# Kernel optimization log

Hardware: AMD Instinct MI355X
Metric: run time of the kernel (lower is better)

The kernel has to match this reference:

```python
import jax, jax.numpy as jnp
import numpy as np

H = 1024
M = 4096
K = 64            # max_memory_updates_per_step
THRESH = 0.5      # surprise_threshold
EPS = 1e-12


def setup_inputs() -> dict:
    key = jax.random.key(0)
    ks = jax.random.split(key, 5)
    B, S = 4, 2048
    return {
        "hidden_states": jax.random.normal(ks[0], (B, S, H), dtype=jnp.float32),
        "ln_gamma": jnp.ones((H,), jnp.float32),
        "ln_beta": jnp.zeros((H,), jnp.float32),
        "Wq": jax.random.normal(ks[1], (H, H), jnp.float32) * 0.02,
        "bq": jnp.zeros((H,), jnp.float32),
        "Wo": jax.random.normal(ks[2], (H, H), jnp.float32) * 0.02,
        "bo": jnp.zeros((H,), jnp.float32),
        "memory": jax.random.normal(ks[3], (M, H), jnp.float32),
        "importance_scores": jax.random.uniform(ks[4], (M,), jnp.float32),
    }


def _layer_norm(x, g, b):
    mu = jnp.mean(x, axis=-1, keepdims=True)
    var = jnp.mean(jnp.square(x - mu), axis=-1, keepdims=True)
    return (x - mu) * jax.lax.rsqrt(var + EPS) * g + b


def reference(hidden_states, ln_gamma, ln_beta, Wq, bq, Wo, bo, memory, importance_scores):
    # LayerNorm
    norm = _layer_norm(hidden_states, ln_gamma, ln_beta)  # [B,S,H]

    # Surprise measure (detached): mean |x| over hidden dim
    surprise = jnp.mean(jnp.abs(jax.lax.stop_gradient(norm)), axis=-1)  # [B,S]

    # --- surprise-based memory update (buffers; no gradient, training mode) ---
    flat_h = jax.lax.stop_gradient(norm).reshape(-1, H)   # [B*S, H]
    flat_s = surprise.reshape(-1)                          # [B*S]
    # top-K surprises, descending (matches where>thr -> sort desc -> take K)
    top_vals, top_idx = jax.lax.top_k(flat_s, K)
    valid = top_vals > THRESH                              # entries below threshold: no write
    # K slots with smallest importance, ascending importance order
    _, slots = jax.lax.top_k(-importance_scores, K)
    new_rows = flat_h[top_idx]                             # [K, H]
    old_rows = memory[slots]                               # [K, H]
    mem = memory.at[slots].set(jnp.where(valid[:, None], new_rows, old_rows))  # [M,H]

    # --- query memory ---
    q = jnp.einsum("bsh,oh->bso", norm, Wq) + bq           # query_proj
    sim = jnp.einsum("bsh,mh->bsm", q, mem)                # [B,S,M]
    attn = jax.nn.softmax(sim, axis=-1)
    retrieved = jnp.einsum("bsm,mh->bsh", attn, mem)       # [B,S,H]
    mem_out = jnp.einsum("bsh,oh->bso", retrieved, Wo) + bo  # output_proj

    # dropout in eval mode = identity; residual add
    return hidden_states + mem_out
```

## Files before the change

### kernel.cpp

```cpp
#include <hip/hip_runtime.h>

#define H 1024
#define MMEM 4096
#define NTOK 8192
#define KTOP 64
#define FTHRESH 0.5f

typedef _Float16 half8 __attribute__((ext_vector_type(8)));
typedef float vf4 __attribute__((ext_vector_type(4)));

__device__ __forceinline__ short f2h(float x){
  union { _Float16 h; short s; } u; u.h = (_Float16)x; return u.s;
}
__device__ __forceinline__ float h2f(short s){
  union { _Float16 h; short s; } u; u.s = s; return (float)u.h;
}
__device__ __forceinline__ unsigned fkey_of(float x){
  unsigned u = __float_as_uint(x);
  return (u & 0x80000000u) ? ~u : (u | 0x80000000u);
}
__device__ __forceinline__ float val_of(unsigned k){
  unsigned u = (k & 0x80000000u) ? (k & 0x7fffffffu) : ~k;
  return __uint_as_float(u);
}

__device__ __forceinline__ void gload_lds16(const short* g, short* l){
  __builtin_amdgcn_global_load_lds(
      (const __attribute__((address_space(1))) unsigned int*)g,
      (__attribute__((address_space(3))) unsigned int*)l, 16, 0, 0);
}

__global__ __launch_bounds__(256) void ln_kernel(
    const float* __restrict__ hs, const float* __restrict__ g, const float* __restrict__ be,
    short* __restrict__ n16, float* __restrict__ surprise)
{
  int row = blockIdx.x, tid = threadIdx.x;
  long base = (long)row * H;
  float4 x = ((const float4*)(hs + base))[tid];
  float s1 = x.x + x.y + x.z + x.w;
  float s2 = x.x*x.x + x.y*x.y + x.z*x.z + x.w*x.w;
  __shared__ float r1[4], r2[4], r3[4];
  int w = tid >> 6, lane = tid & 63;
  for (int o = 32; o; o >>= 1){ s1 += __shfl_down(s1, o); s2 += __shfl_down(s2, o); }
  if (lane == 0){ r1[w] = s1; r2[w] = s2; }
  __syncthreads();
  float S1 = r1[0]+r1[1]+r1[2]+r1[3];
  float S2 = r2[0]+r2[1]+r2[2]+r2[3];
  float mean = S1 * (1.0f/H);
  float var  = S2 * (1.0f/H) - mean*mean;
  float rinv = rsqrtf(var + 1e-12f);
  float4 gg = ((const float4*)g)[tid];
  float4 bb = ((const float4*)be)[tid];
  float4 n;
  n.x = (x.x-mean)*rinv*gg.x + bb.x;
  n.y = (x.y-mean)*rinv*gg.y + bb.y;
  n.z = (x.z-mean)*rinv*gg.z + bb.z;
  n.w = (x.w-mean)*rinv*gg.w + bb.w;
  float sa = fabsf(n.x)+fabsf(n.y)+fabsf(n.z)+fabsf(n.w);
  for (int o = 32; o; o >>= 1) sa += __shfl_down(sa, o);
  if (lane == 0) r3[w] = sa;
  __syncthreads();
  if (tid == 0) surprise[row] = (r3[0]+r3[1]+r3[2]+r3[3]) * (1.0f/H);
  short4 h4;
  h4.x = f2h(n.x); h4.y = f2h(n.y); h4.z = f2h(n.z); h4.w = f2h(n.w);
  ((short4*)(n16 + base))[tid] = h4;
}

__global__ __launch_bounds__(256) void topk_local(
    const float* __restrict__ surprise, const float* __restrict__ imp,
    unsigned long long* __restrict__ cand_s, unsigned long long* __restrict__ cand_i)
{
  __shared__ unsigned long long s[256];
  int b = blockIdx.x, tid = threadIdx.x;
  int maxmode = (b < 32);
  int gidx = maxmode ? (b*256 + tid) : ((b-32)*256 + tid);
  float x = maxmode ? surprise[gidx] : imp[gidx];
  unsigned k = fkey_of(x);
  if (!maxmode) k = ~k;
  s[tid] = ((unsigned long long)k << 32) | (unsigned)(8191 - gidx);
  __syncthreads();
  for (int kk = 2; kk <= 256; kk <<= 1)
    for (int j = kk >> 1; j > 0; j >>= 1){
      int i = tid, ixj = i ^ j;
      if (ixj > i){
        bool asc = ((i & kk) == 0);
        unsigned long long a = s[i], c = s[ixj];
        if ((a < c) == asc){ s[i] = c; s[ixj] = a; }
      }
      __syncthreads();
    }
  if (tid < 64){
    if (maxmode) cand_s[b*64 + tid] = s[tid];
    else         cand_i[(b-32)*64 + tid] = s[tid];
  }
}

__global__ __launch_bounds__(256) void topk_merge(
    const unsigned long long* __restrict__ cand_s, const unsigned long long* __restrict__ cand_i,
    float* __restrict__ top_vals, int* __restrict__ top_idx, int* __restrict__ slots)
{
  __shared__ unsigned long long s[2048];
  int tid = threadIdx.x;
  int N = (blockIdx.x == 0) ? 2048 : 1024;
  const unsigned long long* src = (blockIdx.x == 0) ? cand_s : cand_i;
  for (int i = tid; i < N; i += 256) s[i] = src[i];
  __syncthreads();
  for (int kk = 2; kk <= N; kk <<= 1)
    for (int j = kk >> 1; j > 0; j >>= 1){
      for (int i = tid; i < N; i += 256){
        int ixj = i ^ j;
        if (ixj > i){
          bool asc = ((i & kk) == 0);
          unsigned long long a = s[i], c = s[ixj];
          if ((a < c) == asc){ s[i] = c; s[ixj] = a; }
        }
      }
      __syncthreads();
    }
  if (tid < 64){
    unsigned long long p = s[tid];
    int gi = 8191 - (int)(p & 0xffffffffu);
    if (blockIdx.x == 0){
      top_vals[tid] = val_of((unsigned)(p >> 32));
      top_idx[tid] = gi;
    } else {
      slots[tid] = gi;
    }
  }
}

__global__ __launch_bounds__(256) void prep_all_kernel(
    const float* __restrict__ mem, const float* __restrict__ Wq, const float* __restrict__ Wo,
    const float* __restrict__ bq,
    short* __restrict__ m16, short* __restrict__ wqT, short* __restrict__ wo16,
    float* __restrict__ biasM)
{
  int b = blockIdx.x, tid = threadIdx.x;
  if (b < 4096){
    long i = (long)b * 256 + tid;
    float4 x = ((const float4*)mem)[i];
    short4 h;
    h.x = f2h(x.x); h.y = f2h(x.y); h.z = f2h(x.z); h.w = f2h(x.w);
    ((short4*)m16)[i] = h;
    float4 b4 = ((const float4*)bq)[tid];
    float sb = b4.x*h2f(h.x) + b4.y*h2f(h.y) + b4.z*h2f(h.z) + b4.w*h2f(h.w);
    int wv = tid >> 6, lane = tid & 63;
    for (int o = 32; o; o >>= 1) sb += __shfl_down(sb, o);
    __shared__ float rb_[4];
    if (lane == 0) rb_[wv] = sb;
    __syncthreads();
    if (tid == 0) biasM[b] = rb_[0]+rb_[1]+rb_[2]+rb_[3];
  } else if (b < 5120){
    long i = (long)(b - 4096) * 256 + tid;
    float4 x = ((const float4*)Wo)[i];
    short4 h;
    h.x = f2h(x.x); h.y = f2h(x.y); h.z = f2h(x.z); h.w = f2h(x.w);
    ((short4*)wo16)[i] = h;
  } else {
    __shared__ __align__(16) short t[64][66];
    int tb = b - 5120;
    int r0 = (tb >> 4) * 64, c0 = (tb & 15) * 64;
    #pragma unroll
    for (int k = 0; k < 4; ++k){
      int idx = k*256 + tid;
      int r = idx >> 4, c4 = (idx & 15) * 4;
      float4 x = *(const float4*)&Wq[(long)(r0+r)*H + c0 + c4];
      t[r][c4]   = f2h(x.x);
      t[r][c4+1] = f2h(x.y);
      t[r][c4+2] = f2h(x.z);
      t[r][c4+3] = f2h(x.w);
    }
    __syncthreads();
    #pragma unroll
    for (int k = 0; k < 4; ++k){
      int idx = k*256 + tid;
      int c = idx >> 4, r4 = (idx & 15) * 4;
      short4 h;
      h.x = t[r4][c]; h.y = t[r4+1][c]; h.z = t[r4+2][c]; h.w = t[r4+3][c];
      *(short4*)&wqT[(long)(c0+c)*H + r0 + r4] = h;
    }
  }
}

__global__ __launch_bounds__(256) void update_kernel(
    const float* __restrict__ top_vals, const int* __restrict__ top_idx, const int* __restrict__ slots,
    const float* __restrict__ hs, const float* __restrict__ g, const float* __restrict__ be,
    const float* __restrict__ bq,
    short* __restrict__ m16, float* __restrict__ biasM)
{
  int i = blockIdx.x;
  if (top_vals[i] <= FTHRESH) return;
  int s = slots[i], r = top_idx[i];
  int tid = threadIdx.x, w = tid >> 6, lane = tid & 63;
  long base = (long)r * H;
  float4 x = ((const float4*)(hs + base))[tid];
  float s1 = x.x + x.y + x.z + x.w;
  float s2 = x.x*x.x + x.y*x.y + x.z*x.z + x.w*x.w;
  __shared__ float r1[4], r2[4], rb[4];
  for (int o = 32; o; o >>= 1){ s1 += __shfl_down(s1, o); s2 += __shfl_down(s2, o); }
  if (lane == 0){ r1[w] = s1; r2[w] = s2; }
  __syncthreads();
  float S1 = r1[0]+r1[1]+r1[2]+r1[3];
  float S2 = r2[0]+r2[1]+r2[2]+r2[3];
  float mean = S1 * (1.0f/H);
  float var  = S2 * (1.0f/H) - mean*mean;
  float rinv = rsqrtf(var + 1e-12f);
  float4 gg = ((const float4*)g)[tid];
  float4 bb = ((const float4*)be)[tid];
  short4 h4;
  h4.x = f2h((x.x-mean)*rinv*gg.x + bb.x);
  h4.y = f2h((x.y-mean)*rinv*gg.y + bb.y);
  h4.z = f2h((x.z-mean)*rinv*gg.z + bb.z);
  h4.w = f2h((x.w-mean)*rinv*gg.w + bb.w);
  ((short4*)(m16 + (long)s*H))[tid] = h4;
  float4 b4 = ((const float4*)bq)[tid];
  float sb = b4.x*h2f(h4.x) + b4.y*h2f(h4.y) + b4.z*h2f(h4.z) + b4.w*h2f(h4.w);
  for (int o = 32; o; o >>= 1) sb += __shfl_down(sb, o);
  if (lane == 0) rb[w] = sb;
  __syncthreads();
  if (tid == 0) biasM[s] = rb[0]+rb[1]+rb[2]+rb[3];
}

__global__ __launch_bounds__(256) void gemm_dual(
    const short* __restrict__ A0, const short* __restrict__ B0, int N0, short* __restrict__ O0,
    const short* __restrict__ A1, const short* __restrict__ B1, int N1, short* __restrict__ O1,
    int K)
{
  __shared__ short sA[128*64];
  __shared__ short sB[128*64];
  int tid = threadIdx.x, w = tid >> 6, lane = tid & 63, ln = lane & 15, quad = lane >> 4;
  int wr = w >> 1, wc = w & 1;
  int lin = blockIdx.x;
  int nl  = (lin & 7) * 64 + (lin >> 3);
  int second = (nl >= 256);
  int t = second ? (nl - 256) : nl;
  const short* A = second ? A1 : A0;
  const short* B = second ? B1 : B0;
  short* O = second ? O1 : O0;
  int N = second ? N1 : N0;
  int nwgx = N >> 7;
  long m0 = (long)(t / nwgx) * 128, n0 = (long)(t % nwgx) * 128;
  long Kl = K;
  vf4 acc[4][4];
  #pragma unroll
  for (int i = 0; i < 4; ++i) for (int j = 0; j < 4; ++j) for (int r = 0; r < 4; ++r) acc[i][j][r] = 0.0f;

  for (long kk = 0; kk < Kl; kk += 64){
    #pragma unroll
    for (int j = 0; j < 4; ++j){
      int f = (w*4 + j)*64 + lane;
      int row = f >> 3, c8 = f & 7;
      long go = kk + (long)((c8 ^ (row & 7)) * 8);
      gload_lds16(A + (m0+row)*Kl + go, sA + (w*4+j)*512);
      gload_lds16(B + (n0+row)*Kl + go, sB + (w*4+j)*512);
    }
    __syncthreads();
    #pragma unroll
    for (int ks = 0; ks < 64; ks += 32){
      int cbase = (ks >> 3) + quad;
      half8 bh[4];
      #pragma unroll
      for (int j = 0; j < 4; ++j){
        int rb = wc*64 + j*16 + ln;
        bh[j] = *(const half8*)&sB[rb*64 + (cbase ^ (rb & 7))*8];
      }
      #pragma unroll
      for (int i = 0; i < 4; ++i){
        int ra = wr*64 + i*16 + ln;
        half8 a = *(const half8*)&sA[ra*64 + (cbase ^ (ra & 7))*8];
        #pragma unroll
        for (int j = 0; j < 4; ++j)
          acc[i][j] = __builtin_amdgcn_mfma_f32_16x16x32_f16(a, bh[j], acc[i][j], 0, 0, 0);
      }
    }
    __syncthreads();
  }

  #pragma unroll
  for (int i = 0; i < 4; ++i)
    #pragma unroll
    for (int j = 0; j < 4; ++j)
      #pragma unroll
      for (int r = 0; r < 4; ++r){
        long row = m0 + wr*64 + i*16 + quad*4 + r;
        long col = n0 + wc*64 + j*16 + ln;
        O[row*(long)N + col] = f2h(acc[i][j][r]);
      }
}

template<int MODE>
__global__ __launch_bounds__(512, 2) void gemm256(
    const short* __restrict__ A, const short* __restrict__ B,
    int K, int N,
    short* __restrict__ O1, float* __restrict__ Of,
    const float* __restrict__ resid, const float* __restrict__ biasN)
{
  extern __shared__ short lds[];
  int tid = threadIdx.x, w = tid >> 6, lane = tid & 63, ln = lane & 15, quad = lane >> 4;
  int wr = w >> 2, wc = w & 3;
  int nwgx = gridDim.x, nwg = nwgx * gridDim.y;
  int lin = blockIdx.y * nwgx + blockIdx.x;
  int nl  = (lin & 7) * (nwg >> 3) + (lin >> 3);
  long m0 = (long)(nl / nwgx) * 256, n0 = (long)(nl % nwgx) * 256;
  long Kl = K;
  int NT = K >> 6;

  auto STAGE = [&](const short* __restrict__ G, long rowbase, long kt, short* ldsbase){
    #pragma unroll
    for (int i = 0; i < 2; ++i){
      int f = i*512 + tid;
      int row = f >> 3, c8 = f & 7;
      long go = kt + (long)((c8 ^ (row & 7)) * 8);
      gload_lds16(G + (rowbase + row)*Kl + go, ldsbase + i*4096 + w*512);
    }
  };
  auto LOADA = [&](half8 (&af)[4][2], const short* sAh){
    #pragma unroll
    for (int ks = 0; ks < 2; ++ks){
      int cbase = ks*4 + quad;
      #pragma unroll
      for (int i = 0; i < 4; ++i){
        int ra = wr*64 + i*16 + ln;
        af[i][ks] = *(const half8*)&sAh[ra*64 + (cbase ^ (ra & 7))*8];
      }
    }
  };
  auto LOADB = [&](half8 (&bf)[2][2], const short* sBh){
    #pragma unroll
    for (int ks = 0; ks < 2; ++ks){
      int cbase = ks*4 + quad;
      #pragma unroll
      for (int j = 0; j < 2; ++j){
        int rb = wc*32 + j*16 + ln;
        bf[j][ks] = *(const half8*)&sBh[rb*64 + (cbase ^ (rb & 7))*8];
      }
    }
  };

  vf4 acc[4][4][2];
  #pragma unroll
  for (int p = 0; p < 4; ++p)
    for (int i = 0; i < 4; ++i)
      for (int j = 0; j < 2; ++j)
        for (int r = 0; r < 4; ++r) acc[p][i][j][r] = 0.0f;

  {
    int t1 = (NT > 1) ? 1 : 0;
    STAGE(A, m0 + 0,   0, lds + 0);
    STAGE(B, n0 + 0,   0, lds + 16384);
    STAGE(B, n0 + 128, 0, lds + 16384 + 8192);
    STAGE(A, m0 + 128, 0, lds + 8192);
    STAGE(A, m0 + 0,   (long)t1*64, lds + 32768);
    STAGE(B, n0 + 0,   (long)t1*64, lds + 32768 + 16384);
  }
  asm volatile("s_waitcnt vmcnt(8)" ::: "memory");
  asm volatile("s_barrier" ::: "memory");

  #define PH_MID()  do { \
    asm volatile("s_waitcnt lgkmcnt(0)" ::: "memory"); \
    __builtin_amdgcn_sched_barrier(0); \
    __builtin_amdgcn_s_setprio(1); } while(0)
  #define PH_END() do { \
    __builtin_amdgcn_s_setprio(0); \
    asm volatile("s_waitcnt vmcnt(8)" ::: "memory"); \
    asm volatile("s_barrier" ::: "memory"); } while(0)
  #define MFMA16(ap, af, bf) do { \
    _Pragma("unroll") \
    for (int i = 0; i < 4; ++i){ \
      _Pragma("unroll") \
      for (int j = 0; j < 2; ++j){ \
        ap[i][j] = __builtin_amdgcn_mfma_f32_16x16x32_f16(af[i][0], bf[j][0], ap[i][j], 0, 0, 0); \
        ap[i][j] = __builtin_amdgcn_mfma_f32_16x16x32_f16(af[i][1], bf[j][1], ap[i][j], 0, 0, 0); \
      } \
    } } while(0)

  for (int t = 0; t < NT; ++t){
    int cur = t & 1;
    short* bA = lds + cur*32768;
    short* bB = bA + 16384;
    short* oA = lds + (cur^1)*32768;
    short* oB = oA + 16384;
    int t1 = t + 1; if (t1 >= NT) t1 -= NT;
    int t2 = t + 2; if (t2 >= NT) t2 -= NT;
    long kt1 = (long)t1 * 64, kt2 = (long)t2 * 64;
    half8 af[4][2], bf0[2][2], bf1[2][2];

    LOADA(af, bA);
    LOADB(bf0, bB);
    STAGE(B, n0 + 128, kt1, oB + 8192);
    PH_MID();
    MFMA16(acc[0], af, bf0);
    PH_END();

    LOADB(bf1, bB + 8192);
    STAGE(A, m0 + 128, kt1, oA + 8192);
    PH_MID();
    MFMA16(acc[1], af, bf1);
    PH_END();

    LOADA(af, bA + 8192);
    STAGE(A, m0 + 0, kt2, bA);
    PH_MID();
    MFMA16(acc[2], af, bf0);
    PH_END();

    STAGE(B, n0 + 0, kt2, bB);
    PH_MID();
    MFMA16(acc[3], af, bf1);
    PH_END();
  }
  #undef PH_MID
  #undef PH_END
  #undef MFMA16

  float bn[2][2];
  if (MODE != 2){
    #pragma unroll
    for (int bh = 0; bh < 2; ++bh)
      for (int j = 0; j < 2; ++j)
        bn[bh][j] = biasN[n0 + bh*128 + wc*32 + j*16 + ln];
  }
  #pragma unroll
  for (int p = 0; p < 4; ++p){
    #pragma unroll
    for (int i = 0; i < 4; ++i){
      #pragma unroll
      for (int j = 0; j < 2; ++j){
        #pragma unroll
        for (int r = 0; r < 4; ++r){
          long row = m0 + (p >> 1)*128 + wr*64 + i*16 + quad*4 + r;
          long col = n0 + (p & 1)*128 + wc*32 + j*16 + ln;
          float v = acc[p][i][j][r];
          if (MODE == 1){
            O1[row*(long)N + col] = f2h(v + bn[p & 1][j]);
          } else if (MODE == 2){
            O1[row*(long)N + col] = f2h(v);
          } else {
            Of[row*(long)N + col] = v + resid[row*(long)N + col] + bn[p & 1][j];
          }
        }
      }
    }
  }
}

__global__ __launch_bounds__(512, 2) void gemm_out(
    const short* __restrict__ A, const short* __restrict__ B,
    int K, int N,
    float* __restrict__ Of, const float* __restrict__ resid, const float* __restrict__ biasN)
{
  extern __shared__ short lds[];
  int tid = threadIdx.x, w = tid >> 6, lane = tid & 63, ln = lane & 15, quad = lane >> 4;
  int wr = (w >> 2) & 1, wc = w & 3;
  int nwgx = gridDim.x, nwg = nwgx * gridDim.y;
  int lin = blockIdx.y * nwgx + blockIdx.x;
  int nl  = (lin & 7) * (nwg >> 3) + (lin >> 3);
  long m0 = (long)(nl >> 2) * 128, n0 = (long)(nl & 3) * 256;
  long Kl = K;
  int NT = K >> 6;

  auto STAGE_A = [&](long rowbase, long kt, short* dst){
    int f = tid;
    int row = f >> 3, c8 = f & 7;
    long go = kt + (long)((c8 ^ (row & 7)) * 8);
    gload_lds16(A + (rowbase + row)*Kl + go, dst + w*512);
  };
  auto STAGE_B = [&](long rowbase, long kt, short* dst){
    #pragma unroll
    for (int i = 0; i < 2; ++i){
      int f = i*512 + tid;
      int row = f >> 3, c8 = f & 7;
      long go = kt + (long)((c8 ^ (row & 7)) * 8);
      gload_lds16(B + (rowbase + row)*Kl + go, dst + i*4096 + w*512);
    }
  };
  auto LOADA = [&](half8 (&af)[2][2], const short* sAh){
    #pragma unroll
    for (int ks = 0; ks < 2; ++ks){
      int cbase = ks*4 + quad;
      #pragma unroll
      for (int i = 0; i < 2; ++i){
        int ra = wr*32 + i*16 + ln;
        af[i][ks] = *(const half8*)&sAh[ra*64 + (cbase ^ (ra & 7))*8];
      }
    }
  };
  auto LOADB = [&](half8 (&bf)[2][2], const short* sBh){
    #pragma unroll
    for (int ks = 0; ks < 2; ++ks){
      int cbase = ks*4 + quad;
      #pragma unroll
      for (int j = 0; j < 2; ++j){
        int rb = wc*32 + j*16 + ln;
        bf[j][ks] = *(const half8*)&sBh[rb*64 + (cbase ^ (rb & 7))*8];
      }
    }
  };

  vf4 acc[4][2][2];
  #pragma unroll
  for (int p = 0; p < 4; ++p)
    for (int i = 0; i < 2; ++i)
      for (int j = 0; j < 2; ++j)
        for (int r = 0; r < 4; ++r) acc[p][i][j][r] = 0.0f;

  {
    int t1 = (NT > 1) ? 1 : 0;
    STAGE_A(m0 + 0,   0, lds + 0);
    STAGE_B(n0 + 0,   0, lds + 8192);
    STAGE_B(n0 + 128, 0, lds + 16384);
    STAGE_A(m0 + 64,  0, lds + 4096);
    STAGE_A(m0 + 0,   (long)t1*64, lds + 24576);
    STAGE_B(n0 + 0,   (long)t1*64, lds + 24576+8192);
  }
  asm volatile("s_waitcnt vmcnt(6)" ::: "memory");
  asm volatile("s_barrier" ::: "memory");

  #define FPH_MID()  do { \
    asm volatile("s_waitcnt lgkmcnt(0)" ::: "memory"); \
    __builtin_amdgcn_sched_barrier(0); \
    __builtin_amdgcn_s_setprio(1); } while(0)
  #define FPH_END() do { \
    __builtin_amdgcn_s_setprio(0); \
    asm volatile("s_waitcnt vmcnt(6)" ::: "memory"); \
    asm volatile("s_barrier" ::: "memory"); } while(0)
  #define MFMA8(ap, af, bf) do { \
    _Pragma("unroll") \
    for (int i = 0; i < 2; ++i){ \
      _Pragma("unroll") \
      for (int j = 0; j < 2; ++j){ \
        ap[i][j] = __builtin_amdgcn_mfma_f32_16x16x32_f16(af[i][0], bf[j][0], ap[i][j], 0, 0, 0); \
        ap[i][j] = __builtin_amdgcn_mfma_f32_16x16x32_f16(af[i][1], bf[j][1], ap[i][j], 0, 0, 0); \
      } \
    } } while(0)

  for (int t = 0; t < NT; ++t){
    int cur = t & 1;
    short* bA = lds + cur*24576;
    short* oA = lds + (cur^1)*24576;
    int t1 = t + 1; if (t1 >= NT) t1 -= NT;
    int t2 = t + 2; if (t2 >= NT) t2 -= NT;
    long kt1 = (long)t1 * 64, kt2 = (long)t2 * 64;
    half8 af[2][2], bf0[2][2], bf1[2][2];

    LOADA(af, bA);
    LOADB(bf0, bA + 8192);
    STAGE_B(n0 + 128, kt1, oA + 16384);
    FPH_MID();
    MFMA8(acc[0], af, bf0);
    FPH_END();

    LOADB(bf1, bA + 16384);
    STAGE_A(m0 + 64, kt1, oA + 4096);
    FPH_MID();
    MFMA8(acc[1], af, bf1);
    FPH_END();

    LOADA(af, bA + 4096);
    STAGE_A(m0 + 0, kt2, bA);
    FPH_MID();
    MFMA8(acc[2], af, bf0);
    FPH_END();

    STAGE_B(n0 + 0, kt2, bA + 8192);
    FPH_MID();
    MFMA8(acc[3], af, bf1);
    FPH_END();
  }
  #undef FPH_MID
  #undef FPH_END
  #undef MFMA8

  float bn[2][2];
  #pragma unroll
  for (int bh = 0; bh < 2; ++bh)
    for (int j = 0; j < 2; ++j)
      bn[bh][j] = biasN[n0 + bh*128 + wc*32 + j*16 + ln];
  #pragma unroll
  for (int p = 0; p < 4; ++p){
    #pragma unroll
    for (int i = 0; i < 2; ++i){
      #pragma unroll
      for (int j = 0; j < 2; ++j){
        #pragma unroll
        for (int r = 0; r < 4; ++r){
          long row = m0 + (p >> 1)*64 + wr*32 + i*16 + quad*4 + r;
          long col = n0 + (p & 1)*128 + wc*32 + j*16 + ln;
          Of[row*(long)N + col] = acc[p][i][j][r] + resid[row*(long)N + col] + bn[p & 1][j];
        }
      }
    }
  }
}

__global__ __launch_bounds__(256) void softmax_kernel(short* __restrict__ simP)
{
  long row = blockIdx.x;
  int tid = threadIdx.x, w = tid >> 6, lane = tid & 63;
  half8* ptr = (half8*)(simP + row*MMEM);
  float xf[16];
  float mx = -1e30f;
  #pragma unroll
  for (int j = 0; j < 2; ++j){
    half8 x = ptr[tid + j*256];
    #pragma unroll
    for (int e = 0; e < 8; ++e){ float f = (float)x[e]; xf[j*8+e] = f; mx = fmaxf(mx, f); }
  }
  for (int o = 32; o; o >>= 1) mx = fmaxf(mx, __shfl_xor(mx, o));
  __shared__ float rmax[4], rsum[4];
  if (lane == 0) rmax[w] = mx;
  __syncthreads();
  mx = fmaxf(fmaxf(rmax[0], rmax[1]), fmaxf(rmax[2], rmax[3]));
  float p[16], s = 0.f;
  #pragma unroll
  for (int k = 0; k < 16; ++k){ p[k] = __expf(xf[k] - mx); s += p[k]; }
  for (int o = 32; o; o >>= 1) s += __shfl_xor(s, o);
  if (lane == 0) rsum[w] = s;
  __syncthreads();
  float inv = 1.0f / (rsum[0]+rsum[1]+rsum[2]+rsum[3]);
  #pragma unroll
  for (int j = 0; j < 2; ++j){
    half8 o8;
    #pragma unroll
    for (int e = 0; e < 8; ++e) o8[e] = (_Float16)(p[j*8+e] * inv);
    ptr[tid + j*256] = o8;
  }
}

extern "C" void kernel_launch(void* const* d_in, const int* in_sizes, int n_in,
                              void* d_out, int out_size, void* d_ws, size_t ws_size,
                              hipStream_t stream)
{
  const float* hs  = (const float*)d_in[0];
  const float* gam = (const float*)d_in[1];
  const float* bet = (const float*)d_in[2];
  const float* Wq  = (const float*)d_in[3];
  const float* bq  = (const float*)d_in[4];
  const float* Wo  = (const float*)d_in[5];
  const float* bo  = (const float*)d_in[6];
  const float* mem = (const float*)d_in[7];
  const float* imp = (const float*)d_in[8];
  float* out = (float*)d_out;

  char* ws = (char*)d_ws;
  short* n16   = (short*)(ws);
  short* g16   = (short*)(ws + (16ull<<20));
  short* m16   = (short*)(ws + (32ull<<20));
  short* wqT   = (short*)(ws + (40ull<<20));
  short* simP  = (short*)(ws + (48ull<<20));
  short* vwoT  = (short*)(ws + (112ull<<20));
  short* wo16  = (short*)(ws + (132ull<<20));
  char*  tail  = ws + (134ull<<20);
  float* biasM    = (float*)tail;
  float* surprise = (float*)(tail + (64<<10));
  float* top_vals = (float*)(tail + (128<<10));
  int*   top_idx  = (int*)  (tail + (129<<10));
  int*   slots    = (int*)  (tail + (130<<10));
  unsigned long long* cand_s = (unsigned long long*)(tail + (132<<10));
  unsigned long long* cand_i = (unsigned long long*)(tail + (148<<10));

  static bool attr_done = false;
  if (!attr_done){
    (void)hipFuncSetAttribute(reinterpret_cast<const void*>(&gemm256<1>),
                              hipFuncAttributeMaxDynamicSharedMemorySize, 131072);
    (void)hipFuncSetAttribute(reinterpret_cast<const void*>(&gemm_out),
                              hipFuncAttributeMaxDynamicSharedMemorySize, 98304);
    attr_done = true;
  }

  ln_kernel<<<NTOK, 256, 0, stream>>>(hs, gam, bet, n16, surprise);
  topk_local<<<48, 256, 0, stream>>>(surprise, imp, cand_s, cand_i);
  topk_merge<<<2, 256, 0, stream>>>(cand_s, cand_i, top_vals, top_idx, slots);
  prep_all_kernel<<<5376, 256, 0, stream>>>(mem, Wq, Wo, bq, m16, wqT, wo16, biasM);
  update_kernel<<<KTOP, 256, 0, stream>>>(top_vals, top_idx, slots, hs, gam, bet, bq, m16, biasM);
  gemm_dual<<<512, 256, 0, stream>>>(
      wo16, m16, MMEM, vwoT,  m16, wqT, H, g16,  H);
  gemm256<1><<<dim3(16,32), 512, 131072, stream>>>(
      n16, g16, H, MMEM, simP, nullptr, nullptr, biasM);
  softmax_kernel<<<NTOK, 256, 0, stream>>>(simP);
  gemm_out<<<dim3(4, 64), 512, 98304, stream>>>(
      simP, vwoT, MMEM, H, out, hs, bo);
}
```

Measured before the change: 370.0 us.

## Fuse layernorm and weight-prep kernels; remap gemm256 tiles to XCD-local blocks

Merges the layernorm/surprise kernel and the memory/Wq/Wo fp16 conversion kernel into one launch, dispatching by block index, so one kernel boundary goes away and the two independent streaming jobs can run side by side. It also replaces the gemm256 block remap with an explicit mapping that gives each XCD a contiguous 8x8 group of 256x256 tiles, to improve L2 reuse of the A and B panels. The new mapping hardcodes a 16x32 grid shape.

```diff
diff --git a/kernel.cpp b/kernel.cpp
--- a/kernel.cpp
+++ b/kernel.cpp
@@ -30,40 +30,91 @@
       (__attribute__((address_space(3))) unsigned int*)l, 16, 0, 0);
 }
 
-__global__ __launch_bounds__(256) void ln_kernel(
+__global__ __launch_bounds__(256) void ln_prep_kernel(
     const float* __restrict__ hs, const float* __restrict__ g, const float* __restrict__ be,
-    short* __restrict__ n16, float* __restrict__ surprise)
-{
-  int row = blockIdx.x, tid = threadIdx.x;
-  long base = (long)row * H;
-  float4 x = ((const float4*)(hs + base))[tid];
-  float s1 = x.x + x.y + x.z + x.w;
-  float s2 = x.x*x.x + x.y*x.y + x.z*x.z + x.w*x.w;
-  __shared__ float r1[4], r2[4], r3[4];
-  int w = tid >> 6, lane = tid & 63;
-  for (int o = 32; o; o >>= 1){ s1 += __shfl_down(s1, o); s2 += __shfl_down(s2, o); }
-  if (lane == 0){ r1[w] = s1; r2[w] = s2; }
-  __syncthreads();
-  float S1 = r1[0]+r1[1]+r1[2]+r1[3];
-  float S2 = r2[0]+r2[1]+r2[2]+r2[3];
-  float mean = S1 * (1.0f/H);
-  float var  = S2 * (1.0f/H) - mean*mean;
-  float rinv = rsqrtf(var + 1e-12f);
-  float4 gg = ((const float4*)g)[tid];
-  float4 bb = ((const float4*)be)[tid];
-  float4 n;
-  n.x = (x.x-mean)*rinv*gg.x + bb.x;
-  n.y = (x.y-mean)*rinv*gg.y + bb.y;
-  n.z = (x.z-mean)*rinv*gg.z + bb.z;
-  n.w = (x.w-mean)*rinv*gg.w + bb.w;
-  float sa = fabsf(n.x)+fabsf(n.y)+fabsf(n.z)+fabsf(n.w);
-  for (int o = 32; o; o >>= 1) sa += __shfl_down(sa, o);
-  if (lane == 0) r3[w] = sa;
-  __syncthreads();
-  if (tid == 0) surprise[row] = (r3[0]+r3[1]+r3[2]+r3[3]) * (1.0f/H);
-  short4 h4;
-  h4.x = f2h(n.x); h4.y = f2h(n.y); h4.z = f2h(n.z); h4.w = f2h(n.w);
-  ((short4*)(n16 + base))[tid] = h4;
+    const float* __restrict__ mem, const float* __restrict__ Wq, const float* __restrict__ Wo,
+    const float* __restrict__ bq,
+    short* __restrict__ n16, float* __restrict__ surprise,
+    short* __restrict__ m16, short* __restrict__ wqT, short* __restrict__ wo16,
+    float* __restrict__ biasM)
+{
+  int b = blockIdx.x, tid = threadIdx.x;
+  if (b < NTOK){
+    int row = b;
+    long base = (long)row * H;
+    float4 x = ((const float4*)(hs + base))[tid];
+    float s1 = x.x + x.y + x.z + x.w;
+    float s2 = x.x*x.x + x.y*x.y + x.z*x.z + x.w*x.w;
+    __shared__ float r1[4], r2[4], r3[4];
+    int w = tid >> 6, lane = tid & 63;
+    for (int o = 32; o; o >>= 1){ s1 += __shfl_down(s1, o); s2 += __shfl_down(s2, o); }
+    if (lane == 0){ r1[w] = s1; r2[w] = s2; }
+    __syncthreads();
+    float S1 = r1[0]+r1[1]+r1[2]+r1[3];
+    float S2 = r2[0]+r2[1]+r2[2]+r2[3];
+    float mean = S1 * (1.0f/H);
+    float var  = S2 * (1.0f/H) - mean*mean;
+    float rinv = rsqrtf(var + 1e-12f);
+    float4 gg = ((const float4*)g)[tid];
+    float4 bb = ((const float4*)be)[tid];
+    float4 n;
+    n.x = (x.x-mean)*rinv*gg.x + bb.x;
+    n.y = (x.y-mean)*rinv*gg.y + bb.y;
+    n.z = (x.z-mean)*rinv*gg.z + bb.z;
+    n.w = (x.w-mean)*rinv*gg.w + bb.w;
+    float sa = fabsf(n.x)+fabsf(n.y)+fabsf(n.z)+fabsf(n.w);
+    for (int o = 32; o; o >>= 1) sa += __shfl_down(sa, o);
+    if (lane == 0) r3[w] = sa;
+    __syncthreads();
+    if (tid == 0) surprise[row] = (r3[0]+r3[1]+r3[2]+r3[3]) * (1.0f/H);
+    short4 h4;
+    h4.x = f2h(n.x); h4.y = f2h(n.y); h4.z = f2h(n.z); h4.w = f2h(n.w);
+    ((short4*)(n16 + base))[tid] = h4;
+  } else if (b < NTOK + 4096){
+    int mrow = b - NTOK;
+    long i = (long)mrow * 256 + tid;
+    float4 x = ((const float4*)mem)[i];
+    short4 h;
+    h.x = f2h(x.x); h.y = f2h(x.y); h.z = f2h(x.z); h.w = f2h(x.w);
+    ((short4*)m16)[i] = h;
+    float4 b4 = ((const float4*)bq)[tid];
+    float sb = b4.x*h2f(h.x) + b4.y*h2f(h.y) + b4.z*h2f(h.z) + b4.w*h2f(h.w);
+    int wv = tid >> 6, lane = tid & 63;
+    for (int o = 32; o; o >>= 1) sb += __shfl_down(sb, o);
+    __shared__ float rb_[4];
+    if (lane == 0) rb_[wv] = sb;
+    __syncthreads();
+    if (tid == 0) biasM[mrow] = rb_[0]+rb_[1]+rb_[2]+rb_[3];
+  } else if (b < NTOK + 5120){
+    long i = (long)(b - NTOK - 4096) * 256 + tid;
+    float4 x = ((const float4*)Wo)[i];
+    short4 h;
+    h.x = f2h(x.x); h.y = f2h(x.y); h.z = f2h(x.z); h.w = f2h(x.w);
+    ((short4*)wo16)[i] = h;
+  } else {
+    __shared__ __align__(16) short t[64][66];
+    int tb = b - NTOK - 5120;
+    int r0 = (tb >> 4) * 64, c0 = (tb & 15) * 64;
+    #pragma unroll
+    for (int k = 0; k < 4; ++k){
+      int idx = k*256 + tid;
+      int r = idx >> 4, c4 = (idx & 15) * 4;
+      float4 x = *(const float4*)&Wq[(long)(r0+r)*H + c0 + c4];
+      t[r][c4]   = f2h(x.x);
+      t[r][c4+1] = f2h(x.y);
+      t[r][c4+2] = f2h(x.z);
+      t[r][c4+3] = f2h(x.w);
+    }
+    __syncthreads();
+    #pragma unroll
+    for (int k = 0; k < 4; ++k){
+      int idx = k*256 + tid;
+      int c = idx >> 4, r4 = (idx & 15) * 4;
+      short4 h;
+      h.x = t[r4][c]; h.y = t[r4+1][c]; h.z = t[r4+2][c]; h.w = t[r4+3][c];
+      *(short4*)&wqT[(long)(c0+c)*H + r0 + r4] = h;
+    }
+  }
 }
 
 __global__ __launch_bounds__(256) void topk_local(
@@ -125,59 +176,6 @@
       top_idx[tid] = gi;
     } else {
       slots[tid] = gi;
-    }
-  }
-}
-
-__global__ __launch_bounds__(256) void prep_all_kernel(
-    const float* __restrict__ mem, const float* __restrict__ Wq, const float* __restrict__ Wo,
-    const float* __restrict__ bq,
-    short* __restrict__ m16, short* __restrict__ wqT, short* __restrict__ wo16,
-    float* __restrict__ biasM)
-{
-  int b = blockIdx.x, tid = threadIdx.x;
-  if (b < 4096){
-    long i = (long)b * 256 + tid;
-    float4 x = ((const float4*)mem)[i];
-    short4 h;
-    h.x = f2h(x.x); h.y = f2h(x.y); h.z = f2h(x.z); h.w = f2h(x.w);
-    ((short4*)m16)[i] = h;
-    float4 b4 = ((const float4*)bq)[tid];
-    float sb = b4.x*h2f(h.x) + b4.y*h2f(h.y) + b4.z*h2f(h.z) + b4.w*h2f(h.w);
-    int wv = tid >> 6, lane = tid & 63;
-    for (int o = 32; o; o >>= 1) sb += __shfl_down(sb, o);
-    __shared__ float rb_[4];
-    if (lane == 0) rb_[wv] = sb;
-    __syncthreads();
-    if (tid == 0) biasM[b] = rb_[0]+rb_[1]+rb_[2]+rb_[3];
-  } else if (b < 5120){
-    long i = (long)(b - 4096) * 256 + tid;
-    float4 x = ((const float4*)Wo)[i];
-    short4 h;
-    h.x = f2h(x.x); h.y = f2h(x.y); h.z = f2h(x.z); h.w = f2h(x.w);
-    ((short4*)wo16)[i] = h;
-  } else {
-    __shared__ __align__(16) short t[64][66];
-    int tb = b - 5120;
-    int r0 = (tb >> 4) * 64, c0 = (tb & 15) * 64;
-    #pragma unroll
-    for (int k = 0; k < 4; ++k){
-      int idx = k*256 + tid;
-      int r = idx >> 4, c4 = (idx & 15) * 4;
-      float4 x = *(const float4*)&Wq[(long)(r0+r)*H + c0 + c4];
-      t[r][c4]   = f2h(x.x);
-      t[r][c4+1] = f2h(x.y);
-      t[r][c4+2] = f2h(x.z);
-      t[r][c4+3] = f2h(x.w);
-    }
-    __syncthreads();
-    #pragma unroll
-    for (int k = 0; k < 4; ++k){
-      int idx = k*256 + tid;
-      int c = idx >> 4, r4 = (idx & 15) * 4;
-      short4 h;
-      h.x = t[r4][c]; h.y = t[r4+1][c]; h.z = t[r4+2][c]; h.w = t[r4+3][c];
-      *(short4*)&wqT[(long)(c0+c)*H + r0 + r4] = h;
     }
   }
 }
@@ -298,10 +296,12 @@
   extern __shared__ short lds[];
   int tid = threadIdx.x, w = tid >> 6, lane = tid & 63, ln = lane & 15, quad = lane >> 4;
   int wr = w >> 2, wc = w & 3;
-  int nwgx = gridDim.x, nwg = nwgx * gridDim.y;
+  int nwgx = gridDim.x;
   int lin = blockIdx.y * nwgx + blockIdx.x;
-  int nl  = (lin & 7) * (nwg >> 3) + (lin >> 3);
-  long m0 = (long)(nl / nwgx) * 256, n0 = (long)(nl % nwgx) * 256;
+  int xcd = lin & 7, ii = lin >> 3;
+  int mt = (xcd >> 1)*8 + (ii >> 3);
+  int nt = (xcd & 1)*8 + (ii & 7);
+  long m0 = (long)mt * 256, n0 = (long)nt * 256;
   long Kl = K;
   int NT = K >> 6;
 
@@ -668,10 +668,10 @@
     attr_done = true;
   }
 
-  ln_kernel<<<NTOK, 256, 0, stream>>>(hs, gam, bet, n16, surprise);
+  ln_prep_kernel<<<NTOK + 5376, 256, 0, stream>>>(
+      hs, gam, bet, mem, Wq, Wo, bq, n16, surprise, m16, wqT, wo16, biasM);
   topk_local<<<48, 256, 0, stream>>>(surprise, imp, cand_s, cand_i);
   topk_merge<<<2, 256, 0, stream>>>(cand_s, cand_i, top_vals, top_idx, slots);
-  prep_all_kernel<<<5376, 256, 0, stream>>>(mem, Wq, Wo, bq, m16, wqT, wo16, biasM);
   update_kernel<<<KTOP, 256, 0, stream>>>(top_vals, top_idx, slots, hs, gam, bet, bq, m16, biasM);
   gemm_dual<<<512, 256, 0, stream>>>(
       wo16, m16, MMEM, vwoT,  m16, wqT, H, g16,  H);
```

New measurement: 367.2 us. About the same (-0.8%).
